# Optimization experiments

Hardware: AMD Instinct MI355X
Metric: run time of the kernel (lower is better)

Reference implementation:

```python
import jax, jax.numpy as jnp
import numpy as np

VERY_NEG = -100000000000.0
EPS = 1e-10
PAGERANK_LAMBDA = 0.8
FACT_SCALE = 1.0
B, E, F, LQ = 64, 1000, 4000, 30
T = 100      # trans_units
EMB = 300    # embed_units
WV = 30000   # word vocab
EV = 50007   # entity vocab (+7 specials)
GNN_LAYERS = 2


def linear(x, W, b):
    return x @ W.T + b


def lstm(x, Wih, Whh, bih, bhh):
    # torch nn.LSTM, single layer, batch_first. gate order i,f,g,o
    Bb = x.shape[0]
    H = Whh.shape[1]
    def step(carry, xt):
        h, c = carry
        g = xt @ Wih.T + h @ Whh.T + bih + bhh
        i, f, gg, o = jnp.split(g, 4, axis=-1)
        c = jax.nn.sigmoid(f) * c + jax.nn.sigmoid(i) * jnp.tanh(gg)
        h = jax.nn.sigmoid(o) * jnp.tanh(c)
        return (h, c), h
    init = (jnp.zeros((Bb, H), x.dtype), jnp.zeros((Bb, H), x.dtype))
    (h, _), ys = jax.lax.scan(step, init, jnp.swapaxes(x, 0, 1))
    return jnp.swapaxes(ys, 0, 1), h


def gather_entity(x, head_idx):
    # sparse_bmm(entity2fact_mat, x): each fact row has one nonzero at its head entity
    # x [B,E,D], head_idx [B,F] -> [B,F,D]
    return jnp.take_along_axis(x, head_idx[:, :, None], axis=1)


def scatter_fact(y, tail_idx):
    # sparse_bmm(fact2entity_mat, y): scatter-add fact rows into their tail entity
    # y [B,F,D], tail_idx [B,F] -> [B,E,D]
    Bb, Ff, D = y.shape
    seg = (jnp.arange(Bb)[:, None] * E + tail_idx).reshape(-1)
    return jax.ops.segment_sum(y.reshape(Bb * Ff, D), seg, num_segments=Bb * E).reshape(Bb, E, D)


def forward(word_emb, entity_emb, ent_W, ent_b, lstm_Wih, lstm_Whh, lstm_bih, lstm_bhh,
            q2e_W, q2e_b, e2q_W, e2q_b, e2e_W, e2e_b,
            kbh_W, kbh_b, kbt_W, kbt_b, kbs_W, kbs_b,
            q2e_adj_mat, query_text, local_entity, kb_fact_rel, head_idx, tail_idx):
    div = jnp.sqrt(jnp.asarray(T, jnp.float32))
    query_mask = (query_text != 0).astype(jnp.float32)          # [B,LQ]

    # node encoder (LSTM) over query words
    qw = word_emb[query_text]                                   # [B,LQ,EMB]
    query_hidden_emb, qh = lstm(qw, lstm_Wih, lstm_Whh, lstm_bih, lstm_bhh)
    query_node_emb = qh[:, None, :]                             # [B,1,T]

    local_fact_emb = linear(entity_emb[kb_fact_rel], ent_W, ent_b)     # [B,F,T]
    local_entity_emb = linear(entity_emb[local_entity], ent_W, ent_b)  # [B,E,T]

    # fact <-> query attention (pre-GNN weighting)
    sim = jnp.einsum('blt,bft->blf', query_hidden_emb, local_fact_emb) / div
    sim = jax.nn.softmax(sim + (1.0 - query_mask[:, :, None]) * VERY_NEG, axis=1)
    fact2query_att = jnp.einsum('blf,blt->bft', sim, query_hidden_emb)  # [B,F,T]
    Wsc = jnp.sum(fact2query_att * local_fact_emb, axis=2) / div        # [B,F]
    W_tilde = jnp.exp(Wsc - jnp.max(Wsc, axis=1, keepdims=True))        # [B,F]

    # e2f_softmax = entity2fact^T @ W_tilde : per-entity sum of W_tilde over out-facts
    e2f_softmax = scatter_fact(W_tilde[:, :, None], head_idx)[:, :, 0]
    e2f_softmax = jnp.maximum(e2f_softmax, EPS)                         # [B,E]

    pagerank_f = q2e_adj_mat                                            # [B,E]
    for i in range(GNN_LAYERS):
        next_emb = local_entity_emb
        # question -> entity
        q2e = linear(jnp.broadcast_to(query_node_emb, (B, E, T)), q2e_W[i], q2e_b[i])
        next_emb = jnp.concatenate([next_emb, q2e], axis=2)
        # entity -> fact
        e2f_emb = jax.nn.relu(linear(local_fact_emb, kbs_W[i], kbs_b[i]) +
                              gather_entity(linear(local_entity_emb, kbh_W[i], kbh_b[i]), head_idx))
        e2f_norm = W_tilde[:, :, None] * gather_entity((pagerank_f / e2f_softmax)[:, :, None], head_idx)
        e2f_emb = e2f_emb * e2f_norm                                    # [B,F,T]
        # fact -> entity
        f2e_emb = jax.nn.relu(linear(local_entity_emb, kbs_W[i], kbs_b[i]) +
                              scatter_fact(linear(e2f_emb, kbt_W[i], kbt_b[i]), tail_idx))
        pagerank_f = (PAGERANK_LAMBDA * scatter_fact(e2f_norm, tail_idx)[:, :, 0] +
                      (1.0 - PAGERANK_LAMBDA) * pagerank_f)
        next_emb = jnp.concatenate([next_emb, FACT_SCALE * f2e_emb], axis=2)  # [B,E,3T]
        # entity -> query ; entity -> entity
        query_node_emb = jnp.einsum('be,bet->bt', pagerank_f,
                                    linear(next_emb, e2q_W[i], e2q_b[i]))[:, None, :]
        local_entity_emb = jax.nn.relu(linear(next_emb, e2e_W[i], e2e_b[i]))
    return local_entity_emb, query_node_emb, pagerank_f


def setup_inputs() -> dict:
    key = jax.random.key(0)
    ks = jax.random.split(key, 24)
    def n(k, shape, s=0.05):
        return (jax.random.normal(k, shape) * s).astype(jnp.float32)
    L, K3 = GNN_LAYERS, 3 * T
    inp = {}
    inp['word_emb'] = n(ks[0], (WV, EMB), 1.0)
    inp['entity_emb'] = n(ks[1], (EV, T), 1.0)
    inp['ent_W'] = n(ks[2], (T, T)); inp['ent_b'] = jnp.zeros((T,), jnp.float32)
    inp['lstm_Wih'] = n(ks[3], (4 * T, EMB)); inp['lstm_Whh'] = n(ks[4], (4 * T, T))
    inp['lstm_bih'] = jnp.zeros((4 * T,), jnp.float32)
    inp['lstm_bhh'] = jnp.zeros((4 * T,), jnp.float32)
    inp['q2e_W'] = n(ks[5], (L, T, T)); inp['q2e_b'] = jnp.zeros((L, T), jnp.float32)
    inp['e2q_W'] = n(ks[6], (L, T, K3)); inp['e2q_b'] = jnp.zeros((L, T), jnp.float32)
    inp['e2e_W'] = n(ks[7], (L, T, K3)); inp['e2e_b'] = jnp.zeros((L, T), jnp.float32)
    inp['kbh_W'] = n(ks[8], (L, T, T)); inp['kbh_b'] = jnp.zeros((L, T), jnp.float32)
    inp['kbt_W'] = n(ks[9], (L, T, T)); inp['kbt_b'] = jnp.zeros((L, T), jnp.float32)
    inp['kbs_W'] = n(ks[10], (L, T, T)); inp['kbs_b'] = jnp.zeros((L, T), jnp.float32)
    inp['q2e_adj_mat'] = (jax.random.uniform(ks[11], (B, E)) < 0.05).astype(jnp.float32)
    inp['query_text'] = jax.random.randint(ks[12], (B, LQ), 0, WV)
    inp['local_entity'] = jax.random.randint(ks[13], (B, E), 0, EV)
    inp['kb_fact_rel'] = jax.random.randint(ks[14], (B, F), 0, EV)
    inp['head_idx'] = jax.random.randint(ks[15], (B, F), 0, E)
    inp['tail_idx'] = jax.random.randint(ks[16], (B, F), 0, E)
    return inp


def reference(word_emb, entity_emb, ent_W, ent_b, lstm_Wih, lstm_Whh, lstm_bih, lstm_bhh,
              q2e_W, q2e_b, e2q_W, e2q_b, e2e_W, e2e_b,
              kbh_W, kbh_b, kbt_W, kbt_b, kbs_W, kbs_b,
              q2e_adj_mat, query_text, local_entity, kb_fact_rel, head_idx, tail_idx):
    return forward(word_emb, entity_emb, ent_W, ent_b, lstm_Wih, lstm_Whh, lstm_bih, lstm_bhh,
                   q2e_W, q2e_b, e2q_W, e2q_b, e2e_W, e2e_b,
                   kbh_W, kbh_b, kbt_W, kbt_b, kbs_W, kbs_b,
                   q2e_adj_mat, query_text, local_entity, kb_fact_rel, head_idx, tail_idx)
```

## Files before the change

kernel.cpp:

```cpp
#include <hip/hip_runtime.h>
#include <hip/hip_bf16.h>

#define BB 64
#define EE 1000
#define FF 4000
#define LQ_ 30
#define TT 100
#define EMB_ 300
#define G4 400
#define EV_ 50007
#define VERY_NEG_ (-100000000000.0f)
#define EPS_ 1e-10f

typedef __attribute__((ext_vector_type(8))) short bf16x8;
typedef __attribute__((ext_vector_type(4))) float f32x4;

__device__ __forceinline__ float sigm(float x) { return 1.0f / (1.0f + expf(-x)); }

__device__ __forceinline__ unsigned short f2bf(float v) {
    __hip_bfloat16 h = __float2bfloat16(v);
    return *reinterpret_cast<unsigned short*>(&h);
}
__device__ __forceinline__ float bf2f(unsigned short s) {
    return __uint_as_float((unsigned)s << 16);
}

__global__ void cvt_bf16_kernel(const float* __restrict__ in, unsigned short* __restrict__ out,
                                long n4) {
    long i = (long)blockIdx.x * 256 + threadIdx.x;
    if (i < n4) {
        float4 v = ((const float4*)in)[i];
        ushort4 o;
        o.x = f2bf(v.x); o.y = f2bf(v.y); o.z = f2bf(v.z); o.w = f2bf(v.w);
        ((ushort4*)out)[i] = o;
    }
}

__global__ void transpose_kernel(const float* __restrict__ in, float* __restrict__ out,
                                 int rows, int cols) {
    int i = blockIdx.x * 256 + threadIdx.x;
    if (i < rows * cols) {
        int r = i / cols, c = i % cols;
        out[c * rows + r] = in[i];
    }
}

__global__ __launch_bounds__(256)
void xw_kernel(const float* __restrict__ word_emb, const int* __restrict__ qtext,
               const float* __restrict__ WihT, const float* __restrict__ bih,
               const float* __restrict__ bhh, float* __restrict__ xw) {
    int bs0 = blockIdx.x * 4;
    __shared__ float x[4][EMB_];
    int tid = threadIdx.x;
    for (int i = tid; i < 4 * EMB_; i += 256) {
        int s = i / EMB_, k = i % EMB_;
        x[s][k] = word_emb[(long)qtext[bs0 + s] * EMB_ + k];
    }
    __syncthreads();
    for (int g = tid; g < G4; g += 256) {
        float b0 = bih[g] + bhh[g];
        float a0 = b0, a1 = b0, a2 = b0, a3 = b0;
        #pragma unroll 4
        for (int k = 0; k < EMB_; ++k) {
            float wv = WihT[k * G4 + g];
            a0 += x[0][k] * wv; a1 += x[1][k] * wv;
            a2 += x[2][k] * wv; a3 += x[3][k] * wv;
        }
        xw[(long)(bs0 + 0) * G4 + g] = a0;
        xw[(long)(bs0 + 1) * G4 + g] = a1;
        xw[(long)(bs0 + 2) * G4 + g] = a2;
        xw[(long)(bs0 + 3) * G4 + g] = a3;
    }
}

__global__ __launch_bounds__(512)
void lstm_kernel(const float* __restrict__ xw, const float* __restrict__ Whh,
                 float* __restrict__ qh_emb, float* __restrict__ qnode) {
    int b = blockIdx.x, tid = threadIdx.x;
    __shared__ __align__(16) float hs[TT];
    __shared__ float cs[TT];
    __shared__ float gs[G4];
    float4 w[25];
    if (tid < G4) {
        const float4* wr = (const float4*)(Whh + (long)tid * TT);
        #pragma unroll
        for (int j = 0; j < 25; ++j) w[j] = wr[j];
    }
    if (tid < TT) { hs[tid] = 0.f; cs[tid] = 0.f; }
    __syncthreads();
    for (int s = 0; s < LQ_; ++s) {
        if (tid < G4) {
            const float4* hv4 = (const float4*)hs;
            float a0 = 0.f, a1 = 0.f, a2 = 0.f, a3 = 0.f;
            #pragma unroll
            for (int j = 0; j < 25; ++j) {
                float4 hv = hv4[j];
                a0 += hv.x * w[j].x; a1 += hv.y * w[j].y;
                a2 += hv.z * w[j].z; a3 += hv.w * w[j].w;
            }
            gs[tid] = xw[((long)b * LQ_ + s) * G4 + tid] + (a0 + a1) + (a2 + a3);
        }
        __syncthreads();
        if (tid < TT) {
            float ci = sigm(gs[TT + tid]) * cs[tid] + sigm(gs[tid]) * tanhf(gs[2 * TT + tid]);
            float hi = sigm(gs[3 * TT + tid]) * tanhf(ci);
            cs[tid] = ci;
            hs[tid] = hi;
            qh_emb[((long)b * LQ_ + s) * TT + tid] = hi;
            if (s == LQ_ - 1) qnode[b * TT + tid] = hi;
        }
        __syncthreads();
    }
}

struct GOut {
    const float* W; int wstride;
    const float* bias;
    const float* bscale;
    const unsigned short* addb;
    const float* addf;
    const float* cvec;
    void* Y; int y_bf16; int relu;
};
struct GArgs {
    const void* X; int x_bf16;
    const int* gidx;
    long rows;
    int nw;
    GOut o[3];
};

__global__ __launch_bounds__(256)
void gemm_multi_kernel(GArgs a) {
    __shared__ __align__(16) short sX[64 * 136];
    __shared__ __align__(16) short sW[112 * 136];
    float* sOut = (float*)sW;
    int tid = threadIdx.x;
    long r0 = (long)blockIdx.x * 64;
    for (int i = tid; i < 64 * 25; i += 256) {
        int r = i / 25, c = i % 25;
        long rr = r0 + r;
        ushort4 v; v.x = 0; v.y = 0; v.z = 0; v.w = 0;
        if (rr < a.rows) {
            long xr = a.gidx ? (long)a.gidx[rr] : rr;
            if (a.x_bf16) {
                v = *(const ushort4*)((const unsigned short*)a.X + xr * TT + c * 4);
            } else {
                float4 f = *(const float4*)((const float*)a.X + xr * TT + c * 4);
                v.x = f2bf(f.x); v.y = f2bf(f.y); v.z = f2bf(f.z); v.w = f2bf(f.w);
            }
        }
        *(ushort4*)&sX[r * 136 + c * 4] = v;
    }
    for (int i = tid; i < 64 * 28; i += 256) {
        int r = i / 28, k = TT + i % 28;
        sX[r * 136 + k] = 0;
    }
    int lane = tid & 63, wv = tid >> 6;
    int arow = lane & 15, agrp = lane >> 4;
    int t_lo = lane & 15, r_hi = (lane >> 4) * 4;
    #pragma unroll
    for (int w = 0; w < 3; ++w) {
        if (w >= a.nw) break;
        for (int i = tid; i < 112 * 32; i += 256) {
            int t = i / 32, k = (i % 32) * 4;
            ushort4 v; v.x = 0; v.y = 0; v.z = 0; v.w = 0;
            if (t < TT && k < TT) {
                float4 f = *(const float4*)(a.o[w].W + (long)t * a.o[w].wstride + k);
                v.x = f2bf(f.x); v.y = f2bf(f.y); v.z = f2bf(f.z); v.w = f2bf(f.w);
            }
            *(ushort4*)&sW[t * 136 + k] = v;
        }
        __syncthreads();
        f32x4 acc[7];
        #pragma unroll
        for (int n = 0; n < 7; ++n) acc[n] = (f32x4){0.f, 0.f, 0.f, 0.f};
        #pragma unroll
        for (int kk = 0; kk < 4; ++kk) {
            bf16x8 av = *(const bf16x8*)&sX[(wv * 16 + arow) * 136 + kk * 32 + agrp * 8];
            #pragma unroll
            for (int n = 0; n < 7; ++n) {
                bf16x8 bv = *(const bf16x8*)&sW[(n * 16 + arow) * 136 + kk * 32 + agrp * 8];
                acc[n] = __builtin_amdgcn_mfma_f32_16x16x32_bf16(av, bv, acc[n], 0, 0, 0);
            }
        }
        __syncthreads();
        #pragma unroll
        for (int n = 0; n < 7; ++n) {
            int t = n * 16 + t_lo;
            if (t < TT) {
                #pragma unroll
                for (int j = 0; j < 4; ++j)
                    sOut[(wv * 16 + r_hi + j) * 104 + t] = acc[n][j];
            }
        }
        __syncthreads();
        for (int i = tid; i < 64 * 25; i += 256) {
            int r = i / 25, c = i % 25;
            long rr = r0 + r;
            if (rr < a.rows) {
                float4 v = *(float4*)&sOut[r * 104 + c * 4];
                if (a.o[w].bias) {
                    float bs = a.o[w].bscale ? a.o[w].bscale[rr] : 1.f;
                    float4 bv = *(const float4*)(a.o[w].bias + c * 4);
                    v.x += bv.x * bs; v.y += bv.y * bs; v.z += bv.z * bs; v.w += bv.w * bs;
                }
                if (a.o[w].addb) {
                    ushort4 ad = *(const ushort4*)(a.o[w].addb + rr * TT + c * 4);
                    v.x += bf2f(ad.x); v.y += bf2f(ad.y); v.z += bf2f(ad.z); v.w += bf2f(ad.w);
                }
                if (a.o[w].addf) {
                    float4 ad = *(const float4*)(a.o[w].addf + rr * TT + c * 4);
                    v.x += ad.x; v.y += ad.y; v.z += ad.z; v.w += ad.w;
                }
                if (a.o[w].cvec) {
                    float4 cv = *(const float4*)(a.o[w].cvec + (long)(rr / EE) * TT + c * 4);
                    v.x += cv.x; v.y += cv.y; v.z += cv.z; v.w += cv.w;
                }
                if (a.o[w].relu) {
                    v.x = fmaxf(v.x, 0.f); v.y = fmaxf(v.y, 0.f);
                    v.z = fmaxf(v.z, 0.f); v.w = fmaxf(v.w, 0.f);
                }
                if (a.o[w].y_bf16) {
                    ushort4 ov;
                    ov.x = f2bf(v.x); ov.y = f2bf(v.y); ov.z = f2bf(v.z); ov.w = f2bf(v.w);
                    *(ushort4*)((unsigned short*)a.o[w].Y + rr * TT + c * 4) = ov;
                } else {
                    *(float4*)((float*)a.o[w].Y + rr * TT + c * 4) = v;
                }
            }
        }
        __syncthreads();
    }
}

__global__ __launch_bounds__(128)
void compose_kernel(const float* __restrict__ A, const float* __restrict__ B,
                    const float* __restrict__ ab, const float* __restrict__ bb,
                    float* __restrict__ C, float* __restrict__ cb) {
    int i = blockIdx.x, j = threadIdx.x;
    __shared__ float arow[TT];
    if (j < TT) arow[j] = A[i * TT + j];
    __syncthreads();
    if (j < TT) {
        float acc = 0.f;
        for (int k = 0; k < TT; ++k) acc += arow[k] * B[k * TT + j];
        C[i * TT + j] = acc;
    }
    if (j == 0) {
        float acc = bb[i];
        for (int k = 0; k < TT; ++k) acc += arow[k] * ab[k];
        cb[i] = acc;
    }
}

__global__ __launch_bounds__(256)
void wsc_kernel(const float* __restrict__ qh_emb, const int* __restrict__ qtext,
                const unsigned short* __restrict__ ent_f, const int* __restrict__ rel,
                float* __restrict__ Wsc) {
    int b = blockIdx.x >> 4;
    int chunk = blockIdx.x & 15;
    __shared__ __align__(16) float qh[LQ_ * TT];
    __shared__ float msk[LQ_];
    for (int i = threadIdx.x; i < LQ_ * TT; i += 256) qh[i] = qh_emb[(long)b * LQ_ * TT + i];
    for (int i = threadIdx.x; i < LQ_; i += 256)
        msk[i] = (qtext[b * LQ_ + i] != 0) ? 0.f : VERY_NEG_;
    __syncthreads();
    int f = chunk * 256 + threadIdx.x;
    if (f >= FF) return;
    long bf = (long)b * FF + f;
    const unsigned short* fr = ent_f + (long)rel[bf] * TT;
    float sim[LQ_];
    #pragma unroll
    for (int l = 0; l < LQ_; ++l) sim[l] = 0.f;
    for (int kq = 0; kq < 25; ++kq) {
        ushort4 x4 = *(const ushort4*)(fr + kq * 4);
        float x0 = bf2f(x4.x), x1 = bf2f(x4.y), x2 = bf2f(x4.z), x3 = bf2f(x4.w);
        #pragma unroll
        for (int l = 0; l < LQ_; ++l) {
            float4 q = ((const float4*)(qh + l * TT))[kq];
            sim[l] += x0 * q.x + x1 * q.y + x2 * q.z + x3 * q.w;
        }
    }
    float mx = -INFINITY;
    #pragma unroll
    for (int l = 0; l < LQ_; ++l) {
        sim[l] *= 0.1f;
        mx = fmaxf(mx, sim[l] + msk[l]);
    }
    float ssum = 0.f, wsum = 0.f;
    #pragma unroll
    for (int l = 0; l < LQ_; ++l) {
        float p = expf(sim[l] + msk[l] - mx);
        ssum += p;
        wsum += p * sim[l];
    }
    Wsc[bf] = wsum / ssum;
}

__global__ __launch_bounds__(256)
void rowmax_kernel(const float* __restrict__ Wsc, float* __restrict__ bmax) {
    int b = blockIdx.x, tid = threadIdx.x;
    __shared__ float red[256];
    float m = -INFINITY;
    for (int f = tid; f < FF; f += 256) m = fmaxf(m, Wsc[(long)b * FF + f]);
    red[tid] = m;
    __syncthreads();
    for (int s = 128; s; s >>= 1) {
        if (tid < s) red[tid] = fmaxf(red[tid], red[tid + s]);
        __syncthreads();
    }
    if (tid == 0) bmax[b] = red[0];
}

__global__ __launch_bounds__(256)
void wtilde_kernel(const float* __restrict__ Wsc, const float* __restrict__ bmax,
                   const int* __restrict__ head, const int* __restrict__ tail,
                   float* __restrict__ W_tilde, float* __restrict__ e2f_sm,
                   float* __restrict__ cnt) {
    int idx = blockIdx.x * 256 + threadIdx.x;
    if (idx >= BB * FF) return;
    int b = idx / FF;
    float wt = expf(Wsc[idx] - bmax[b]);
    W_tilde[idx] = wt;
    atomicAdd(&e2f_sm[(long)b * EE + head[idx]], wt);
    atomicAdd(&cnt[(long)b * EE + tail[idx]], 1.f);
}

__global__ __launch_bounds__(256)
void scan_kernel(const float* __restrict__ cnt, int* __restrict__ offs) {
    int b = blockIdx.x, tid = threadIdx.x;
    __shared__ int ls[256];
    int c0 = 0, c1 = 0, c2 = 0, c3 = 0;
    int start = tid * 4;
    if (start + 0 < EE) c0 = (int)cnt[(long)b * EE + start + 0];
    if (start + 1 < EE) c1 = (int)cnt[(long)b * EE + start + 1];
    if (start + 2 < EE) c2 = (int)cnt[(long)b * EE + start + 2];
    if (start + 3 < EE) c3 = (int)cnt[(long)b * EE + start + 3];
    int s = c0 + c1 + c2 + c3;
    ls[tid] = s;
    __syncthreads();
    for (int d = 1; d < 256; d <<= 1) {
        int v = (tid >= d) ? ls[tid - d] : 0;
        __syncthreads();
        ls[tid] += v;
        __syncthreads();
    }
    int excl = ls[tid] - s + b * FF;
    if (start + 0 < EE) { offs[(long)b * EE + start + 0] = excl; excl += c0; }
    if (start + 1 < EE) { offs[(long)b * EE + start + 1] = excl; excl += c1; }
    if (start + 2 < EE) { offs[(long)b * EE + start + 2] = excl; excl += c2; }
    if (start + 3 < EE) { offs[(long)b * EE + start + 3] = excl; excl += c3; }
    if (b == BB - 1 && tid == 255) offs[BB * EE] = BB * FF;
}

__global__ __launch_bounds__(256)
void sortfacts_kernel(const int* __restrict__ tail, const int* __restrict__ offs,
                      int* __restrict__ fillc, int* __restrict__ perm) {
    int idx = blockIdx.x * 256 + threadIdx.x;
    if (idx >= BB * FF) return;
    int b = idx / FF;
    int bin = b * EE + tail[idx];
    int pos = offs[bin] + atomicAdd(&fillc[bin], 1);
    perm[pos] = idx;
}

__global__ __launch_bounds__(256)
void e2f_sorted_kernel(const unsigned short* __restrict__ kbs_tab,
                       const unsigned short* __restrict__ kbh,
                       const float* __restrict__ W_tilde, const float* __restrict__ pr,
                       const float* __restrict__ e2f_sm,
                       const int* __restrict__ rel, const int* __restrict__ head,
                       const int* __restrict__ offs, const int* __restrict__ perm,
                       unsigned short* __restrict__ eaccb, float* __restrict__ pr_acc) {
    int grp = threadIdx.x >> 7;
    int t = threadIdx.x & 127;
    int bin = blockIdx.x * 2 + grp;
    if (bin >= BB * EE) return;
    int b = bin / EE;
    int j0 = offs[bin], j1 = offs[bin + 1];
    float acc = 0.f, nsum = 0.f;
    for (int j = j0; j < j1; ++j) {
        int f = perm[j];
        long bh = (long)b * EE + head[f];
        float n = W_tilde[f] * pr[bh] / fmaxf(e2f_sm[bh], EPS_);
        if (n != 0.f) {
            nsum += n;
            if (t < TT) {
                float v = bf2f(kbs_tab[(long)rel[f] * TT + t]) + bf2f(kbh[bh * TT + t]);
                acc += fmaxf(v, 0.f) * n;
            }
        }
    }
    if (t < TT) eaccb[(long)bin * TT + t] = f2bf(acc);
    if (t == TT) pr_acc[bin] = nsum;
}

__global__ void pr_update_kernel(const float* __restrict__ pr_acc, float* __restrict__ pr,
                                 float* __restrict__ out2) {
    int i = blockIdx.x * 256 + threadIdx.x;
    if (i < BB * EE) {
        float v = 0.8f * pr_acc[i] + 0.2f * pr[i];
        pr[i] = v;
        if (out2) out2[i] = v;
    }
}

#define RCH 50
__global__ __launch_bounds__(128)
void reduce_kernel(const float* __restrict__ pr, const unsigned short* __restrict__ ent,
                   const int* __restrict__ gidx, const unsigned short* __restrict__ f2e,
                   float* __restrict__ s1, float* __restrict__ s3, float* __restrict__ prsum) {
    int b = blockIdx.x / (EE / RCH), ch = blockIdx.x % (EE / RCH);
    int e0 = ch * RCH, tid = threadIdx.x;
    __shared__ float prl[RCH];
    __shared__ long erow[RCH];
    if (tid < RCH) {
        long idx = (long)b * EE + e0 + tid;
        prl[tid] = pr[idx];
        erow[tid] = gidx ? (long)gidx[idx] : idx;
    }
    __syncthreads();
    if (tid == 0) {
        float s = 0.f;
        for (int e = 0; e < RCH; ++e) s += prl[e];
        if (s != 0.f) atomicAdd(&prsum[b], s);
    }
    if (tid < TT) {
        float a1 = 0.f, a3 = 0.f;
        for (int e = 0; e < RCH; ++e) {
            float p = prl[e];
            if (p != 0.f) {
                a1 += p * bf2f(ent[erow[e] * TT + tid]);
                a3 += p * bf2f(f2e[((long)b * EE + e0 + e) * TT + tid]);
            }
        }
        atomicAdd(&s1[b * TT + tid], a1);
        atomicAdd(&s3[b * TT + tid], a3);
    }
}

__global__ __launch_bounds__(128)
void qvec_kernel(const float* __restrict__ qnode,
                 const float* __restrict__ q2eW, const float* __restrict__ q2eb,
                 const float* __restrict__ e2eW, const float* __restrict__ e2eb,
                 const float* __restrict__ e2qW, const float* __restrict__ e2qb,
                 float* __restrict__ q2e_vec, float* __restrict__ cvec_e2e,
                 float* __restrict__ cvec_e2q) {
    int b = blockIdx.x, t = threadIdx.x;
    __shared__ float qn[TT], qv[TT];
    if (t < TT) qn[t] = qnode[b * TT + t];
    __syncthreads();
    if (t < TT) {
        float acc = q2eb[t];
        for (int k = 0; k < TT; ++k) acc += qn[k] * q2eW[t * TT + k];
        qv[t] = acc;
        q2e_vec[b * TT + t] = acc;
    }
    __syncthreads();
    if (t < TT) {
        float a1 = e2eb[t], a2 = e2qb[t];
        for (int k = 0; k < TT; ++k) {
            a1 += qv[k] * e2eW[(long)t * 300 + TT + k];
            a2 += qv[k] * e2qW[(long)t * 300 + TT + k];
        }
        cvec_e2e[b * TT + t] = a1;
        cvec_e2q[b * TT + t] = a2;
    }
}

__global__ __launch_bounds__(128)
void qnode_kernel(const float* __restrict__ s1, const float* __restrict__ s3,
                  const float* __restrict__ prsum, const float* __restrict__ cvec_e2q,
                  const float* __restrict__ e2qW, float* __restrict__ qnode,
                  float* __restrict__ out2) {
    int b = blockIdx.x, t = threadIdx.x;
    __shared__ float s1l[TT], s3l[TT];
    if (t < TT) { s1l[t] = s1[b * TT + t]; s3l[t] = s3[b * TT + t]; }
    __syncthreads();
    if (t < TT) {
        float acc = prsum[b] * cvec_e2q[b * TT + t];
        const float* wr = e2qW + (long)t * 300;
        for (int k = 0; k < TT; ++k) acc += s1l[k] * wr[k] + s3l[k] * wr[200 + k];
        qnode[b * TT + t] = acc;
        if (out2) out2[b * TT + t] = acc;
    }
}

extern "C" void kernel_launch(void* const* d_in, const int* in_sizes, int n_in,
                              void* d_out, int out_size, void* d_ws, size_t ws_size,
                              hipStream_t stream) {
    const float* word_emb   = (const float*)d_in[0];
    const float* entity_emb = (const float*)d_in[1];
    const float* ent_W      = (const float*)d_in[2];
    const float* ent_b      = (const float*)d_in[3];
    const float* lstm_Wih   = (const float*)d_in[4];
    const float* lstm_Whh   = (const float*)d_in[5];
    const float* lstm_bih   = (const float*)d_in[6];
    const float* lstm_bhh   = (const float*)d_in[7];
    const float* q2e_W      = (const float*)d_in[8];
    const float* q2e_b      = (const float*)d_in[9];
    const float* e2q_W      = (const float*)d_in[10];
    const float* e2q_b      = (const float*)d_in[11];
    const float* e2e_W      = (const float*)d_in[12];
    const float* e2e_b      = (const float*)d_in[13];
    const float* kbh_W      = (const float*)d_in[14];
    const float* kbh_b      = (const float*)d_in[15];
    const float* kbt_W      = (const float*)d_in[16];
    const float* kbt_b      = (const float*)d_in[17];
    const float* kbs_W      = (const float*)d_in[18];
    const float* kbs_b      = (const float*)d_in[19];
    const float* q2e_adj    = (const float*)d_in[20];
    const int* query_text   = (const int*)d_in[21];
    const int* local_entity = (const int*)d_in[22];
    const int* kb_fact_rel  = (const int*)d_in[23];
    const int* head_idx     = (const int*)d_in[24];
    const int* tail_idx     = (const int*)d_in[25];
    float* out = (float*)d_out;

    char* base = (char*)d_ws;
    size_t off = 0;
    auto alloc = [&](size_t bytes) {
        void* p = base + off;
        off = (off + bytes + 255) & ~(size_t)255;
        return p;
    };
    const size_t NE = (size_t)BB * EE;
    unsigned short* emb_bf  = (unsigned short*)alloc((size_t)EV_ * TT * 2);
    unsigned short* ent_f   = (unsigned short*)alloc((size_t)EV_ * TT * 2);
    unsigned short* kbs0    = (unsigned short*)alloc((size_t)EV_ * TT * 2);
    unsigned short* kbs1    = (unsigned short*)alloc((size_t)EV_ * TT * 2);
    unsigned short* entB    = (unsigned short*)alloc(NE * TT * 2);
    unsigned short* kbh_bf  = (unsigned short*)alloc(NE * TT * 2);
    unsigned short* kbs_e   = (unsigned short*)alloc(NE * TT * 2);
    unsigned short* tmp     = (unsigned short*)alloc(NE * TT * 2);
    unsigned short* eaccb   = (unsigned short*)alloc(NE * TT * 2);
    float* pr_acc           = (float*)alloc(NE * 4);
    float* xw               = (float*)alloc((size_t)BB * LQ_ * G4 * 4);
    float* qh_emb           = (float*)alloc((size_t)BB * LQ_ * TT * 4);
    float* WihT             = (float*)alloc((size_t)G4 * EMB_ * 4);
    float* Wsc              = (float*)alloc((size_t)BB * FF * 4);
    float* W_tilde          = (float*)alloc((size_t)BB * FF * 4);
    float* bmaxb            = (float*)alloc(BB * 4);
    float* e2f_sm           = (float*)alloc(NE * 4);
    float* cnt              = (float*)alloc(NE * 4);
    float* pr               = (float*)alloc(NE * 4);
    float* qnode            = (float*)alloc((size_t)BB * TT * 4);
    float* q2e_vec          = (float*)alloc((size_t)BB * TT * 4);
    float* cvec_e2e         = (float*)alloc((size_t)BB * TT * 4);
    float* cvec_e2q         = (float*)alloc((size_t)BB * TT * 4);
    float* s1               = (float*)alloc((size_t)BB * TT * 4);
    float* s3               = (float*)alloc((size_t)BB * TT * 4);
    float* prsum            = (float*)alloc(BB * 4);
    float* Ckbs0            = (float*)alloc((size_t)TT * TT * 4);
    float* Ckbs1            = (float*)alloc((size_t)TT * TT * 4);
    float* cb0              = (float*)alloc(TT * 4);
    float* cb1              = (float*)alloc(TT * 4);
    int* offs               = (int*)alloc((NE + 1) * 4);
    int* fillc              = (int*)alloc(NE * 4);
    int* perm               = (int*)alloc((size_t)BB * FF * 4);
    unsigned short* f2e = kbh_bf;

    transpose_kernel<<<(G4 * EMB_ + 255) / 256, 256, 0, stream>>>(lstm_Wih, WihT, G4, EMB_);
    xw_kernel<<<BB * LQ_ / 4, 256, 0, stream>>>(word_emb, query_text, WihT, lstm_bih, lstm_bhh, xw);
    lstm_kernel<<<BB, 512, 0, stream>>>(xw, lstm_Whh, qh_emb, qnode);

    cvt_bf16_kernel<<<(EV_ * TT / 4 + 255) / 256, 256, 0, stream>>>(entity_emb, emb_bf,
                                                                    (long)EV_ * TT / 4);
    compose_kernel<<<TT, 128, 0, stream>>>(kbs_W, ent_W, ent_b, kbs_b, Ckbs0, cb0);
    compose_kernel<<<TT, 128, 0, stream>>>(kbs_W + TT * TT, ent_W, ent_b, kbs_b + TT,
                                           Ckbs1, cb1);
    {
        GArgs g{};
        g.X = emb_bf; g.x_bf16 = 1; g.gidx = nullptr; g.rows = EV_; g.nw = 3;
        g.o[0].W = ent_W; g.o[0].wstride = TT; g.o[0].bias = ent_b;
        g.o[0].Y = ent_f; g.o[0].y_bf16 = 1;
        g.o[1].W = Ckbs0; g.o[1].wstride = TT; g.o[1].bias = cb0;
        g.o[1].Y = kbs0; g.o[1].y_bf16 = 1;
        g.o[2].W = Ckbs1; g.o[2].wstride = TT; g.o[2].bias = cb1;
        g.o[2].Y = kbs1; g.o[2].y_bf16 = 1;
        gemm_multi_kernel<<<(EV_ + 63) / 64, 256, 0, stream>>>(g);
    }

    wsc_kernel<<<BB * 16, 256, 0, stream>>>(qh_emb, query_text, ent_f, kb_fact_rel, Wsc);
    rowmax_kernel<<<BB, 256, 0, stream>>>(Wsc, bmaxb);
    hipMemsetAsync(e2f_sm, 0, 2 * NE * 4, stream);
    wtilde_kernel<<<(BB * FF + 255) / 256, 256, 0, stream>>>(Wsc, bmaxb, head_idx, tail_idx,
                                                             W_tilde, e2f_sm, cnt);
    hipMemcpyAsync(pr, q2e_adj, NE * 4, hipMemcpyDeviceToDevice, stream);

    scan_kernel<<<BB, 256, 0, stream>>>(cnt, offs);
    hipMemsetAsync(fillc, 0, NE * 4, stream);
    sortfacts_kernel<<<(BB * FF + 255) / 256, 256, 0, stream>>>(tail_idx, offs, fillc, perm);

    for (int i = 0; i < 2; ++i) {
        const unsigned short* kbs_tab = i ? kbs1 : kbs0;
        qvec_kernel<<<BB, 128, 0, stream>>>(qnode, q2e_W + i * TT * TT, q2e_b + i * TT,
                                            e2e_W + i * TT * 300, e2e_b + i * TT,
                                            e2q_W + i * TT * 300, e2q_b + i * TT,
                                            q2e_vec, cvec_e2e, cvec_e2q);
        {
            GArgs g{};
            g.X = i ? (const void*)entB : (const void*)ent_f;
            g.x_bf16 = 1;
            g.gidx = i ? nullptr : local_entity;
            g.rows = (long)NE; g.nw = 3;
            g.o[0].W = kbh_W + i * TT * TT; g.o[0].wstride = TT; g.o[0].bias = kbh_b + i * TT;
            g.o[0].Y = kbh_bf; g.o[0].y_bf16 = 1;
            g.o[1].W = kbs_W + i * TT * TT; g.o[1].wstride = TT; g.o[1].bias = kbs_b + i * TT;
            g.o[1].Y = kbs_e; g.o[1].y_bf16 = 1;
            g.o[2].W = e2e_W + i * TT * 300; g.o[2].wstride = 300;
            g.o[2].Y = tmp; g.o[2].y_bf16 = 1;
            gemm_multi_kernel<<<(int)(NE / 64), 256, 0, stream>>>(g);
        }
        e2f_sorted_kernel<<<(int)(NE / 2), 256, 0, stream>>>(
            kbs_tab, kbh_bf, W_tilde, pr, e2f_sm, kb_fact_rel, head_idx, offs, perm,
            eaccb, pr_acc);
        {
            GArgs g{};
            g.X = eaccb; g.x_bf16 = 1; g.gidx = nullptr; g.rows = (long)NE; g.nw = 1;
            g.o[0].W = kbt_W + i * TT * TT; g.o[0].wstride = TT;
            g.o[0].bias = kbt_b + i * TT; g.o[0].bscale = cnt;
            g.o[0].addb = kbs_e;
            g.o[0].Y = (void*)f2e; g.o[0].y_bf16 = 1; g.o[0].relu = 1;
            gemm_multi_kernel<<<(int)(NE / 64), 256, 0, stream>>>(g);
        }
        pr_update_kernel<<<(int)((NE + 255) / 256), 256, 0, stream>>>(
            pr_acc, pr, (i == 1) ? out + 6406400 : nullptr);
        hipMemsetAsync(s1, 0, (size_t)(2 * BB * TT + BB) * 4, stream);
        reduce_kernel<<<BB * (EE / RCH), 128, 0, stream>>>(
            pr, i ? entB : ent_f, i ? nullptr : local_entity, f2e, s1, s3, prsum);
        qnode_kernel<<<BB, 128, 0, stream>>>(s1, s3, prsum, cvec_e2q, e2q_W + i * TT * 300,
                                             qnode, (i == 1) ? out + 6400000 : nullptr);
        {
            GArgs g{};
            g.X = f2e; g.x_bf16 = 1; g.gidx = nullptr; g.rows = (long)NE; g.nw = 1;
            g.o[0].W = e2e_W + i * TT * 300 + 200; g.o[0].wstride = 300;
            g.o[0].addb = tmp; g.o[0].cvec = cvec_e2e; g.o[0].relu = 1;
            g.o[0].Y = i ? (void*)out : (void*)entB; g.o[0].y_bf16 = i ? 0 : 1;
            gemm_multi_kernel<<<(int)(NE / 64), 256, 0, stream>>>(g);
        }
    }
}
```

Before: 844.4 us.

## Presort fact metadata, fuse pagerank update into e2f kernel, unroll fact loop

The sort kernel now writes per-fact (relation, head-row) pairs and a precomputed W_tilde/e2f_sm weight in sorted order, so the e2f kernel reads contiguous data instead of chasing perm indirection into several arrays. The pagerank blend is folded into the e2f kernel using ping-pong pr buffers, which removes the separate pr_update launch and the pr_acc buffer. The inner fact loop is unrolled by two to expose more independent loads. The cost is extra writes during the one-time sort and a more complex loop body.

```diff
diff --git a/kernel.cpp b/kernel.cpp
--- a/kernel.cpp
+++ b/kernel.cpp
@@ -355,54 +355,67 @@
 }
 
 __global__ __launch_bounds__(256)
-void sortfacts_kernel(const int* __restrict__ tail, const int* __restrict__ offs,
-                      int* __restrict__ fillc, int* __restrict__ perm) {
+void sortfacts_kernel(const int* __restrict__ tail, const int* __restrict__ head,
+                      const int* __restrict__ rel, const float* __restrict__ W_tilde,
+                      const float* __restrict__ e2f_sm, const int* __restrict__ offs,
+                      int* __restrict__ fillc, int2* __restrict__ rh_perm,
+                      float* __restrict__ wsm_perm) {
     int idx = blockIdx.x * 256 + threadIdx.x;
     if (idx >= BB * FF) return;
     int b = idx / FF;
     int bin = b * EE + tail[idx];
     int pos = offs[bin] + atomicAdd(&fillc[bin], 1);
-    perm[pos] = idx;
+    int bh = b * EE + head[idx];
+    rh_perm[pos] = make_int2(rel[idx], bh);
+    wsm_perm[pos] = W_tilde[idx] / fmaxf(e2f_sm[bh], EPS_);
 }
 
 __global__ __launch_bounds__(256)
 void e2f_sorted_kernel(const unsigned short* __restrict__ kbs_tab,
                        const unsigned short* __restrict__ kbh,
-                       const float* __restrict__ W_tilde, const float* __restrict__ pr,
-                       const float* __restrict__ e2f_sm,
-                       const int* __restrict__ rel, const int* __restrict__ head,
-                       const int* __restrict__ offs, const int* __restrict__ perm,
-                       unsigned short* __restrict__ eaccb, float* __restrict__ pr_acc) {
+                       const float* __restrict__ wsm_perm, const int2* __restrict__ rh_perm,
+                       const float* __restrict__ pr_cur, const int* __restrict__ offs,
+                       unsigned short* __restrict__ eaccb, float* __restrict__ pr_nxt,
+                       float* __restrict__ pr_out) {
     int grp = threadIdx.x >> 7;
     int t = threadIdx.x & 127;
     int bin = blockIdx.x * 2 + grp;
-    if (bin >= BB * EE) return;
-    int b = bin / EE;
     int j0 = offs[bin], j1 = offs[bin + 1];
     float acc = 0.f, nsum = 0.f;
-    for (int j = j0; j < j1; ++j) {
-        int f = perm[j];
-        long bh = (long)b * EE + head[f];
-        float n = W_tilde[f] * pr[bh] / fmaxf(e2f_sm[bh], EPS_);
-        if (n != 0.f) {
-            nsum += n;
+    int j = j0;
+    for (; j + 2 <= j1; j += 2) {
+        float w0 = wsm_perm[j], w1 = wsm_perm[j + 1];
+        int2 rh0 = rh_perm[j];
+        int2 rh1 = rh_perm[j + 1];
+        float n0 = w0 * pr_cur[rh0.y];
+        float n1 = w1 * pr_cur[rh1.y];
+        nsum += n0 + n1;
+        if ((n0 != 0.f) || (n1 != 0.f)) {
             if (t < TT) {
-                float v = bf2f(kbs_tab[(long)rel[f] * TT + t]) + bf2f(kbh[bh * TT + t]);
-                acc += fmaxf(v, 0.f) * n;
-            }
+                float v0 = fmaxf(bf2f(kbs_tab[(long)rh0.x * TT + t]) +
+                                 bf2f(kbh[(long)rh0.y * TT + t]), 0.f);
+                float v1 = fmaxf(bf2f(kbs_tab[(long)rh1.x * TT + t]) +
+                                 bf2f(kbh[(long)rh1.y * TT + t]), 0.f);
+                acc += v0 * n0 + v1 * n1;
+            }
+        }
+    }
+    if (j < j1) {
+        float w0 = wsm_perm[j];
+        int2 rh0 = rh_perm[j];
+        float n0 = w0 * pr_cur[rh0.y];
+        nsum += n0;
+        if (n0 != 0.f && t < TT) {
+            float v0 = fmaxf(bf2f(kbs_tab[(long)rh0.x * TT + t]) +
+                             bf2f(kbh[(long)rh0.y * TT + t]), 0.f);
+            acc += v0 * n0;
         }
     }
     if (t < TT) eaccb[(long)bin * TT + t] = f2bf(acc);
-    if (t == TT) pr_acc[bin] = nsum;
-}
-
-__global__ void pr_update_kernel(const float* __restrict__ pr_acc, float* __restrict__ pr,
-                                 float* __restrict__ out2) {
-    int i = blockIdx.x * 256 + threadIdx.x;
-    if (i < BB * EE) {
-        float v = 0.8f * pr_acc[i] + 0.2f * pr[i];
-        pr[i] = v;
-        if (out2) out2[i] = v;
+    if (t == TT) {
+        float pv = 0.8f * nsum + 0.2f * pr_cur[bin];
+        pr_nxt[bin] = pv;
+        if (pr_out) pr_out[bin] = pv;
     }
 }
 
@@ -535,7 +548,6 @@
     unsigned short* kbs_e   = (unsigned short*)alloc(NE * TT * 2);
     unsigned short* tmp     = (unsigned short*)alloc(NE * TT * 2);
     unsigned short* eaccb   = (unsigned short*)alloc(NE * TT * 2);
-    float* pr_acc           = (float*)alloc(NE * 4);
     float* xw               = (float*)alloc((size_t)BB * LQ_ * G4 * 4);
     float* qh_emb           = (float*)alloc((size_t)BB * LQ_ * TT * 4);
     float* WihT             = (float*)alloc((size_t)G4 * EMB_ * 4);
@@ -544,7 +556,8 @@
     float* bmaxb            = (float*)alloc(BB * 4);
     float* e2f_sm           = (float*)alloc(NE * 4);
     float* cnt              = (float*)alloc(NE * 4);
-    float* pr               = (float*)alloc(NE * 4);
+    float* prA              = (float*)alloc(NE * 4);
+    float* prB              = (float*)alloc(NE * 4);
     float* qnode            = (float*)alloc((size_t)BB * TT * 4);
     float* q2e_vec          = (float*)alloc((size_t)BB * TT * 4);
     float* cvec_e2e         = (float*)alloc((size_t)BB * TT * 4);
@@ -558,7 +571,8 @@
     float* cb1              = (float*)alloc(TT * 4);
     int* offs               = (int*)alloc((NE + 1) * 4);
     int* fillc              = (int*)alloc(NE * 4);
-    int* perm               = (int*)alloc((size_t)BB * FF * 4);
+    int2* rh_perm           = (int2*)alloc((size_t)BB * FF * 8);
+    float* wsm_perm         = (float*)alloc((size_t)BB * FF * 4);
     unsigned short* f2e = kbh_bf;
 
     transpose_kernel<<<(G4 * EMB_ + 255) / 256, 256, 0, stream>>>(lstm_Wih, WihT, G4, EMB_);
@@ -587,14 +601,17 @@
     hipMemsetAsync(e2f_sm, 0, 2 * NE * 4, stream);
     wtilde_kernel<<<(BB * FF + 255) / 256, 256, 0, stream>>>(Wsc, bmaxb, head_idx, tail_idx,
                                                              W_tilde, e2f_sm, cnt);
-    hipMemcpyAsync(pr, q2e_adj, NE * 4, hipMemcpyDeviceToDevice, stream);
+    hipMemcpyAsync(prA, q2e_adj, NE * 4, hipMemcpyDeviceToDevice, stream);
 
     scan_kernel<<<BB, 256, 0, stream>>>(cnt, offs);
     hipMemsetAsync(fillc, 0, NE * 4, stream);
-    sortfacts_kernel<<<(BB * FF + 255) / 256, 256, 0, stream>>>(tail_idx, offs, fillc, perm);
+    sortfacts_kernel<<<(BB * FF + 255) / 256, 256, 0, stream>>>(
+        tail_idx, head_idx, kb_fact_rel, W_tilde, e2f_sm, offs, fillc, rh_perm, wsm_perm);
 
     for (int i = 0; i < 2; ++i) {
         const unsigned short* kbs_tab = i ? kbs1 : kbs0;
+        float* pr_cur = i ? prB : prA;
+        float* pr_nxt = i ? prA : prB;
         qvec_kernel<<<BB, 128, 0, stream>>>(qnode, q2e_W + i * TT * TT, q2e_b + i * TT,
                                             e2e_W + i * TT * 300, e2e_b + i * TT,
                                             e2q_W + i * TT * 300, e2q_b + i * TT,
@@ -614,8 +631,8 @@
             gemm_multi_kernel<<<(int)(NE / 64), 256, 0, stream>>>(g);
         }
         e2f_sorted_kernel<<<(int)(NE / 2), 256, 0, stream>>>(
-            kbs_tab, kbh_bf, W_tilde, pr, e2f_sm, kb_fact_rel, head_idx, offs, perm,
-            eaccb, pr_acc);
+            kbs_tab, kbh_bf, wsm_perm, rh_perm, pr_cur, offs,
+            eaccb, pr_nxt, (i == 1) ? out + 6406400 : nullptr);
         {
             GArgs g{};
             g.X = eaccb; g.x_bf16 = 1; g.gidx = nullptr; g.rows = (long)NE; g.nw = 1;
@@ -625,11 +642,9 @@
             g.o[0].Y = (void*)f2e; g.o[0].y_bf16 = 1; g.o[0].relu = 1;
             gemm_multi_kernel<<<(int)(NE / 64), 256, 0, stream>>>(g);
         }
-        pr_update_kernel<<<(int)((NE + 255) / 256), 256, 0, stream>>>(
-            pr_acc, pr, (i == 1) ? out + 6406400 : nullptr);
         hipMemsetAsync(s1, 0, (size_t)(2 * BB * TT + BB) * 4, stream);
         reduce_kernel<<<BB * (EE / RCH), 128, 0, stream>>>(
-            pr, i ? entB : ent_f, i ? nullptr : local_entity, f2e, s1, s3, prsum);
+            pr_nxt, i ? entB : ent_f, i ? nullptr : local_entity, f2e, s1, s3, prsum);
         qnode_kernel<<<BB, 128, 0, stream>>>(s1, s3, prsum, cvec_e2q, e2q_W + i * TT * 300,
                                              qnode, (i == 1) ? out + 6400000 : nullptr);
         {
```

Measured after the change: 781.4 us. 7.5% less time.
